# Performance work log

Measured on AMD Instinct MI355X. Metric: run time of the kernel, lower is better.

## Reference

```python
import jax, jax.numpy as jnp
import numpy as np

# Constants matching the module / repo call convention:
# self.tensor2points(x, self.voxel_size) -> offset := init voxel_size, voxel_size := default
OFFSET = np.array([0.1, 0.1, 0.2], dtype=np.float32)      # init_kwargs voxel_size (used as offset)
VOX    = np.array([0.05, 0.05, 0.1], dtype=np.float32)    # tensor2points default voxel_size
BIG = 1e10  # cross-batch distance sentinel


def setup_inputs() -> dict:
    key = jax.random.key(0)
    k1, k2, k3, k4, k5 = jax.random.split(key, 5)
    m, n, C = 4096, 32768, 64
    # sparse voxel indices: (batch, z, y, x) over KITTI grid [40, 1600, 1408]
    zi = jax.random.randint(k1, (m, 1), 0, 40, dtype=jnp.int32)
    yi = jax.random.randint(k2, (m, 1), 0, 1600, dtype=jnp.int32)
    xi = jax.random.randint(k3, (m, 1), 0, 1408, dtype=jnp.int32)
    bi = jnp.zeros((m, 1), dtype=jnp.int32)
    x_indices = jnp.concatenate([bi, zi, yi, xi], axis=1)
    x_features = jax.random.normal(k4, (m, C), dtype=jnp.float32)
    # unknown points: bxyz in KITTI range x:[0,70.4] y:[-40,40] z:[-3,1]
    u = jax.random.uniform(k5, (n, 3), dtype=jnp.float32)
    lo = jnp.array([0.0, -40.0, -3.0], dtype=jnp.float32)
    hi = jnp.array([70.4, 40.0, 1.0], dtype=jnp.float32)
    xyz = lo + u * (hi - lo)
    points_mean = jnp.concatenate([jnp.zeros((n, 1), jnp.float32), xyz], axis=1)
    return {"x_features": x_features, "x_indices": x_indices, "points_mean": points_mean}


def reference(x_features, x_indices, points_mean):
    # tensor2points: voxel index (b,z,y,x) -> world bxyz
    idxf = x_indices.astype(jnp.float32)
    vox = jnp.asarray(VOX)
    off = jnp.asarray(OFFSET)
    known_xyz = idxf[:, jnp.array([3, 2, 1])] * vox + off + 0.5 * vox   # (m,3)
    known_b = idxf[:, 0]                                                # (m,)
    unk_b = points_mean[:, 0]                                           # (n,)
    unk_xyz = points_mean[:, 1:4]                                       # (n,3)
    # brute-force squared distances (pointnet2 three_nn returns squared dists)
    d2 = jnp.sum((unk_xyz[:, None, :] - known_xyz[None, :, :]) ** 2, axis=-1)  # (n,m)
    d2 = jnp.where(unk_b[:, None] == known_b[None, :], d2, jnp.float32(BIG))
    neg, idx = jax.lax.top_k(-d2, 3)        # 3 nearest neighbors
    dist = -neg                              # (n,3)
    dist_recip = 1.0 / (dist + 1e-8)
    weight = dist_recip / jnp.sum(dist_recip, axis=1, keepdims=True)    # (n,3)
    # three_interpolate: gather + weighted sum
    interpolated = jnp.sum(x_features[idx] * weight[..., None], axis=1)  # (n,C)
    return interpolated
```

## Files before the change

kernel.cpp:

```cpp
#include <hip/hip_runtime.h>


#define NXC 24
#define NYC 27
#define NCC (NXC * NYC)
#define WCELL 3.0f
#define NBB 16

__device__ __forceinline__ void ins_lex(float d, int j,
                                        float& a0, float& a1, float& a2,
                                        int& i0, int& i1, int& i2) {
    bool c0 = (d < a0) || (d == a0 && j < i0);
    bool c1 = (d < a1) || (d == a1 && j < i1);
    bool c2 = (d < a2) || (d == a2 && j < i2);
    float nb1 = c0 ? a0 : (c1 ? d : a1);
    int   nj1 = c0 ? i0 : (c1 ? j : i1);
    float nb2 = c1 ? a1 : (c2 ? d : a2);
    int   nj2 = c1 ? i1 : (c2 ? j : i2);
    a0 = c0 ? d : a0; i0 = c0 ? j : i0;
    a1 = nb1; i1 = nj1; a2 = nb2; i2 = nj2;
}

__device__ __forceinline__ int kcell_of(int4 v) {
    float kx = ((float)v.w * 0.05f + 0.1f) + 0.025f;
    float ky = ((float)v.z * 0.05f + 0.1f) + 0.025f;
    int ix = min(NXC - 1, max(0, (int)(kx * (1.0f / WCELL))));
    int iy = min(NYC - 1, max(0, (int)(ky * (1.0f / WCELL))));
    return iy * NXC + ix;
}

__device__ __forceinline__ int qcell_of(float qx, float qy) {
    int ix = min(NXC - 1, max(0, (int)floorf(qx * (1.0f / WCELL))));
    int iy = min(NYC - 1, max(0, (int)floorf(qy * (1.0f / WCELL))));
    return iy * NXC + ix;
}

__global__ __launch_bounds__(1024) void prep_fused(const int4* __restrict__ xind4,
                                                   const float* __restrict__ pts,
                                                   float4* __restrict__ tab,
                                                   float4* __restrict__ qpts,
                                                   int* __restrict__ cs_g,
                                                   int m, int n) {
#pragma clang fp contract(off)
    __shared__ int hAK[NCC], hAQ[NCC];
    __shared__ int hPK[NCC], hPQ[NCC];
    __shared__ int bk[NCC], bq[NCC];
    __shared__ int wsk[16], wsq[16];
    const int t = threadIdx.x, b = blockIdx.x;
    for (int i = t; i < NCC; i += 1024) { hAK[i] = 0; hAQ[i] = 0; hPK[i] = 0; hPQ[i] = 0; }
    __syncthreads();

    const int tot = m + n;
    const int chunk = (tot + NBB - 1) / NBB;
    const int e0 = b * chunk;
    const int e1 = min(e0 + chunk, tot);

    for (int base = 0; base < m; base += 4096) {
        int4 v[4];
#pragma unroll
        for (int k = 0; k < 4; ++k) {
            int j = base + k * 1024 + t;
            v[k] = xind4[min(j, m - 1)];
        }
#pragma unroll
        for (int k = 0; k < 4; ++k) {
            int j = base + k * 1024 + t;
            if (j < m) {
                int cell = kcell_of(v[k]);
                atomicAdd(&hAK[cell], 1);
                if (j < e0) atomicAdd(&hPK[cell], 1);
            }
        }
    }
    for (int base = 0; base < n; base += 4096) {
        float4 u[4];
#pragma unroll
        for (int k = 0; k < 4; ++k) {
            int qi = base + k * 1024 + t;
            u[k] = ((const float4*)pts)[min(qi, n - 1)];
        }
#pragma unroll
        for (int k = 0; k < 4; ++k) {
            int qi = base + k * 1024 + t;
            if (qi < n) {
                int cell = qcell_of(u[k].y, u[k].z);
                atomicAdd(&hAQ[cell], 1);
                if (m + qi < e0) atomicAdd(&hPQ[cell], 1);
            }
        }
    }
    __syncthreads();

    int ownK = 0, ownQ = 0, vk = 0, vq = 0;
    if (t < NCC) { ownK = hAK[t]; ownQ = hAQ[t]; vk = ownK; vq = ownQ; }
#pragma unroll
    for (int d = 1; d < 64; d <<= 1) {
        int ok = __shfl_up(vk, d, 64);
        int oq = __shfl_up(vq, d, 64);
        if ((t & 63) >= d) { vk += ok; vq += oq; }
    }
    if ((t & 63) == 63) { wsk[t >> 6] = vk; wsq[t >> 6] = vq; }
    __syncthreads();
    if (t < 64) {
        int ok0 = (t < 16) ? wsk[t] : 0;
        int oq0 = (t < 16) ? wsq[t] : 0;
        int sk = ok0, sq = oq0;
#pragma unroll
        for (int d = 1; d < 16; d <<= 1) {
            int ok = __shfl_up(sk, d, 64);
            int oq = __shfl_up(sq, d, 64);
            if (t >= d) { sk += ok; sq += oq; }
        }
        if (t < 16) { wsk[t] = sk - ok0; wsq[t] = sq - oq0; }
    }
    __syncthreads();
    if (t < NCC) {
        int exK = vk + wsk[t >> 6] - ownK;
        int exQ = vq + wsq[t >> 6] - ownQ;
        bk[t] = exK + hPK[t];
        bq[t] = exQ + hPQ[t];
        if (b == 0) cs_g[t] = exK;
    }
    if (b == 0 && t == 0) cs_g[NCC] = m;
    __syncthreads();

    for (int i = t; i < NCC; i += 1024) { hPK[i] = 0; hPQ[i] = 0; }
    __syncthreads();

    for (int e = e0 + t; e < e1; e += 1024) {
        if (e < m) {
            int4 v = xind4[e];
            float kx = ((float)v.w * 0.05f + 0.1f) + 0.025f;
            float ky = ((float)v.z * 0.05f + 0.1f) + 0.025f;
            float kz = ((float)v.y * 0.1f  + 0.2f) + 0.05f;
            int cell = kcell_of(v);
            int r = atomicAdd(&hPK[cell], 1);
            tab[bk[cell] + r] = make_float4(kx, ky, kz, __int_as_float(e));
        } else {
            int q = e - m;
            float4 u = ((const float4*)pts)[q];
            int cell = qcell_of(u.y, u.z);
            int r = atomicAdd(&hPQ[cell], 1);
            qpts[bq[cell] + r] = make_float4(__int_as_float(q), u.y, u.z, u.w);
        }
    }
}

__global__ __launch_bounds__(256) void scan3nn(const float4* __restrict__ tab,
                                               const int* __restrict__ cs,
                                               const float4* __restrict__ qpts,
                                               const float* __restrict__ feats,
                                               float* __restrict__ out,
                                               int m, int n, int C) {
#pragma clang fp contract(off)
    __shared__ int cs_lds[NCC + 1];
    const int t = threadIdx.x;
    for (int i = t; i < NCC + 1; i += 256) cs_lds[i] = cs[i];
    __syncthreads();

    const int sub = t & 3;
    const int gid = blockIdx.x * 64 + (t >> 2);
    const float INF = __builtin_huge_valf();
    if (gid >= n) return;

    const float4 rec = qpts[gid];
    const int q = __float_as_int(rec.x);
    const float qx = rec.y, qy = rec.z, qz = rec.w;

    float a0 = INF, a1 = INF, a2 = INF;
    int   i0 = 0x7fffffff, i1 = 0x7fffffff, i2 = 0x7fffffff;
    float T = INF;

    const int cx = min(NXC - 1, max(0, (int)floorf(qx * (1.0f / WCELL))));
    const int cy = min(NYC - 1, max(0, (int)floorf(qy * (1.0f / WCELL))));

    auto scan_span = [&](int s0, int s1) {
        for (int s = s0 + sub; s < s1; s += 4) {
            float4 kp = tab[s];
            float dx = qx - kp.x, dy = qy - kp.y, dz = qz - kp.z;
            float d = dx * dx + dy * dy;
            d = d + dz * dz;
            ins_lex(d, __float_as_int(kp.w), a0, a1, a2, i0, i1, i2);
        }
    };
    auto tighten = [&]() {
        float tg = a2;
        tg = fminf(tg, __shfl_xor(tg, 1, 4));
        tg = fminf(tg, __shfl_xor(tg, 2, 4));
        T = tg;
    };
    auto row_mdy2 = [&](int iy) {
        float cyl = (float)iy * WCELL;
        float mdy = fmaxf(fmaxf(cyl - qy, qy - (cyl + WCELL)), 0.f);
        return mdy * mdy;
    };
    auto row_scan = [&](int iy, int excl_lo, int excl_hi) -> bool {
        float mdy2 = row_mdy2(iy);
        float Ts = T * 1.0001f + 1e-4f;
        if (mdy2 > Ts) return false;
        float rem = fmaxf(Ts - mdy2, 0.f);
        float rx = fminf(sqrtf(rem), 1000.0f);
        int ixlo = max(0, (int)floorf((qx - rx) * (1.0f / WCELL)) - 1);
        int ixhi = min(NXC - 1, (int)floorf((qx + rx) * (1.0f / WCELL)) + 1);
        const int rowb = iy * NXC;
        if (excl_lo <= excl_hi) {
            int h1 = min(ixhi, excl_lo - 1);
            if (ixlo <= h1) scan_span(cs_lds[rowb + ixlo], cs_lds[rowb + h1 + 1]);
            int l2 = max(ixlo, excl_hi + 1);
            if (l2 <= ixhi) scan_span(cs_lds[rowb + l2], cs_lds[rowb + ixhi + 1]);
        } else {
            scan_span(cs_lds[rowb + ixlo], cs_lds[rowb + ixhi + 1]);
        }
        tighten();
        return true;
    };

    const int lo0 = max(0, cx - 1), hi0 = min(NXC - 1, cx + 1);
    scan_span(cs_lds[cy * NXC + lo0], cs_lds[cy * NXC + hi0 + 1]);
    tighten();
    row_scan(cy, lo0, hi0);
    bool up = true, dn = true;
    for (int o = 1; (up || dn) && o < NYC; ++o) {
        if (up) { int iy = cy + o; up = (iy < NYC) && row_scan(iy, 1, 0); }
        if (dn) { int iy = cy - o; dn = (iy >= 0) && row_scan(iy, 1, 0); }
    }

    for (int mlane = 1; mlane < 4; mlane <<= 1) {
        float b0 = __shfl_xor(a0, mlane, 4);
        float b1 = __shfl_xor(a1, mlane, 4);
        float b2 = __shfl_xor(a2, mlane, 4);
        int   j0 = __shfl_xor(i0, mlane, 4);
        int   j1 = __shfl_xor(i1, mlane, 4);
        int   j2 = __shfl_xor(i2, mlane, 4);
        ins_lex(b0, j0, a0, a1, a2, i0, i1, i2);
        ins_lex(b1, j1, a0, a1, a2, i0, i1, i2);
        ins_lex(b2, j2, a0, a1, a2, i0, i1, i2);
    }

    float r0 = 1.0f / (a0 + 1e-8f);
    float r1 = 1.0f / (a1 + 1e-8f);
    float r2 = 1.0f / (a2 + 1e-8f);
    float s  = r0 + r1 + r2;
    const float w0 = r0 / s, w1 = r1 / s, w2 = r2 / s;

    const int nf4 = C >> 2;
    const float4* F  = (const float4*)feats;
    const float4* F0 = F + (size_t)min(i0, m - 1) * nf4;
    const float4* F1 = F + (size_t)min(i1, m - 1) * nf4;
    const float4* F2 = F + (size_t)min(i2, m - 1) * nf4;
    float4* O = (float4*)out + (size_t)q * nf4;
    for (int c = sub; c < nf4; c += 4) {
        float4 a = F0[c], b = F1[c], cc = F2[c];
        float4 o;
        o.x = w0 * a.x + w1 * b.x + w2 * cc.x;
        o.y = w0 * a.y + w1 * b.y + w2 * cc.y;
        o.z = w0 * a.z + w1 * b.z + w2 * cc.z;
        o.w = w0 * a.w + w1 * b.w + w2 * cc.w;
        O[c] = o;
    }
}

extern "C" void kernel_launch(void* const* d_in, const int* in_sizes, int n_in,
                              void* d_out, int out_size, void* d_ws, size_t ws_size,
                              hipStream_t stream) {
    const float* feats = (const float*)d_in[0];
    const int4*  xind4 = (const int4*)d_in[1];
    const float* pts   = (const float*)d_in[2];
    float*       out   = (float*)d_out;

    const int m = in_sizes[1] / 4;
    const int n = in_sizes[2] / 4;
    const int C = in_sizes[0] / m;

    const size_t off_tab  = 0;
    const size_t off_cs   = off_tab  + (size_t)m * 16;
    const size_t off_qpts = off_cs   + (size_t)(NCC + 1) * 4;
    const size_t need     = off_qpts + (size_t)n * 16;

    if (ws_size >= need && m >= 3 && (C & 3) == 0) {
        char* ws = (char*)d_ws;
        float4* tab  = (float4*)(ws + off_tab);
        int*    cs   = (int*)(ws + off_cs);
        float4* qpts = (float4*)(ws + off_qpts);

        prep_fused<<<NBB, 1024, 0, stream>>>(xind4, pts, tab, qpts, cs, m, n);
        const int nb = (n + 63) / 64;
        scan3nn<<<nb, 256, 0, stream>>>(tab, cs, qpts, feats, out, m, n, C);
    }
}
```

Baseline: 42.55 us.

## Pack histogram counters into one atomic and use 8 lanes per query

The prep kernel now packs the total and prefix cell counts into a single 32-bit LDS atomic (low and high 16 bits) when m and n are below 65536, which halves the atomics in the histogram pass. The query histogram loop is unrolled to 8 loads per thread. The search kernel splits each query across 8 lanes instead of 4, with 32 queries per block, and widens the shuffles to match. More lanes per query adds parallelism and grid size but also adds shuffle and merge overhead, and lanes go idle when cells hold few points.

```diff
diff --git a/kernel.cpp b/kernel.cpp
--- a/kernel.cpp
+++ b/kernel.cpp
@@ -35,6 +35,7 @@
     return iy * NXC + ix;
 }
 
+template <bool PACKED>
 __global__ __launch_bounds__(1024) void prep_fused(const int4* __restrict__ xind4,
                                                    const float* __restrict__ pts,
                                                    float4* __restrict__ tab,
@@ -42,12 +43,12 @@
                                                    int* __restrict__ cs_g,
                                                    int m, int n) {
 #pragma clang fp contract(off)
-    __shared__ int hAK[NCC], hAQ[NCC];
+    __shared__ int hK[NCC], hQ[NCC];
     __shared__ int hPK[NCC], hPQ[NCC];
     __shared__ int bk[NCC], bq[NCC];
     __shared__ int wsk[16], wsq[16];
     const int t = threadIdx.x, b = blockIdx.x;
-    for (int i = t; i < NCC; i += 1024) { hAK[i] = 0; hAQ[i] = 0; hPK[i] = 0; hPQ[i] = 0; }
+    for (int i = t; i < NCC; i += 1024) { hK[i] = 0; hQ[i] = 0; hPK[i] = 0; hPQ[i] = 0; }
     __syncthreads();
 
     const int tot = m + n;
@@ -67,32 +68,49 @@
             int j = base + k * 1024 + t;
             if (j < m) {
                 int cell = kcell_of(v[k]);
-                atomicAdd(&hAK[cell], 1);
-                if (j < e0) atomicAdd(&hPK[cell], 1);
+                if constexpr (PACKED) {
+                    atomicAdd(&hK[cell], (j < e0) ? 0x10001 : 1);
+                } else {
+                    atomicAdd(&hK[cell], 1);
+                    if (j < e0) atomicAdd(&hPK[cell], 1);
+                }
             }
         }
     }
-    for (int base = 0; base < n; base += 4096) {
-        float4 u[4];
-#pragma unroll
-        for (int k = 0; k < 4; ++k) {
+    for (int base = 0; base < n; base += 8192) {
+        float4 u[8];
+#pragma unroll
+        for (int k = 0; k < 8; ++k) {
             int qi = base + k * 1024 + t;
             u[k] = ((const float4*)pts)[min(qi, n - 1)];
         }
 #pragma unroll
-        for (int k = 0; k < 4; ++k) {
+        for (int k = 0; k < 8; ++k) {
             int qi = base + k * 1024 + t;
             if (qi < n) {
                 int cell = qcell_of(u[k].y, u[k].z);
-                atomicAdd(&hAQ[cell], 1);
-                if (m + qi < e0) atomicAdd(&hPQ[cell], 1);
+                if constexpr (PACKED) {
+                    atomicAdd(&hQ[cell], (m + qi < e0) ? 0x10001 : 1);
+                } else {
+                    atomicAdd(&hQ[cell], 1);
+                    if (m + qi < e0) atomicAdd(&hPQ[cell], 1);
+                }
             }
         }
     }
     __syncthreads();
 
-    int ownK = 0, ownQ = 0, vk = 0, vq = 0;
-    if (t < NCC) { ownK = hAK[t]; ownQ = hAQ[t]; vk = ownK; vq = ownQ; }
+    int ownK = 0, ownQ = 0, preK = 0, preQ = 0, vk = 0, vq = 0;
+    if (t < NCC) {
+        if constexpr (PACKED) {
+            ownK = hK[t] & 0xffff;  preK = ((unsigned)hK[t]) >> 16;
+            ownQ = hQ[t] & 0xffff;  preQ = ((unsigned)hQ[t]) >> 16;
+        } else {
+            ownK = hK[t]; preK = hPK[t];
+            ownQ = hQ[t]; preQ = hPQ[t];
+        }
+        vk = ownK; vq = ownQ;
+    }
 #pragma unroll
     for (int d = 1; d < 64; d <<= 1) {
         int ok = __shfl_up(vk, d, 64);
@@ -117,8 +135,8 @@
     if (t < NCC) {
         int exK = vk + wsk[t >> 6] - ownK;
         int exQ = vq + wsq[t >> 6] - ownQ;
-        bk[t] = exK + hPK[t];
-        bq[t] = exQ + hPQ[t];
+        bk[t] = exK + preK;
+        bq[t] = exQ + preQ;
         if (b == 0) cs_g[t] = exK;
     }
     if (b == 0 && t == 0) cs_g[NCC] = m;
@@ -158,8 +176,8 @@
     for (int i = t; i < NCC + 1; i += 256) cs_lds[i] = cs[i];
     __syncthreads();
 
-    const int sub = t & 3;
-    const int gid = blockIdx.x * 64 + (t >> 2);
+    const int sub = t & 7;
+    const int gid = blockIdx.x * 32 + (t >> 3);
     const float INF = __builtin_huge_valf();
     if (gid >= n) return;
 
@@ -175,7 +193,7 @@
     const int cy = min(NYC - 1, max(0, (int)floorf(qy * (1.0f / WCELL))));
 
     auto scan_span = [&](int s0, int s1) {
-        for (int s = s0 + sub; s < s1; s += 4) {
+        for (int s = s0 + sub; s < s1; s += 8) {
             float4 kp = tab[s];
             float dx = qx - kp.x, dy = qy - kp.y, dz = qz - kp.z;
             float d = dx * dx + dy * dy;
@@ -185,8 +203,9 @@
     };
     auto tighten = [&]() {
         float tg = a2;
-        tg = fminf(tg, __shfl_xor(tg, 1, 4));
-        tg = fminf(tg, __shfl_xor(tg, 2, 4));
+        tg = fminf(tg, __shfl_xor(tg, 1, 8));
+        tg = fminf(tg, __shfl_xor(tg, 2, 8));
+        tg = fminf(tg, __shfl_xor(tg, 4, 8));
         T = tg;
     };
     auto row_mdy2 = [&](int iy) {
@@ -225,13 +244,13 @@
         if (dn) { int iy = cy - o; dn = (iy >= 0) && row_scan(iy, 1, 0); }
     }
 
-    for (int mlane = 1; mlane < 4; mlane <<= 1) {
-        float b0 = __shfl_xor(a0, mlane, 4);
-        float b1 = __shfl_xor(a1, mlane, 4);
-        float b2 = __shfl_xor(a2, mlane, 4);
-        int   j0 = __shfl_xor(i0, mlane, 4);
-        int   j1 = __shfl_xor(i1, mlane, 4);
-        int   j2 = __shfl_xor(i2, mlane, 4);
+    for (int mlane = 1; mlane < 8; mlane <<= 1) {
+        float b0 = __shfl_xor(a0, mlane, 8);
+        float b1 = __shfl_xor(a1, mlane, 8);
+        float b2 = __shfl_xor(a2, mlane, 8);
+        int   j0 = __shfl_xor(i0, mlane, 8);
+        int   j1 = __shfl_xor(i1, mlane, 8);
+        int   j2 = __shfl_xor(i2, mlane, 8);
         ins_lex(b0, j0, a0, a1, a2, i0, i1, i2);
         ins_lex(b1, j1, a0, a1, a2, i0, i1, i2);
         ins_lex(b2, j2, a0, a1, a2, i0, i1, i2);
@@ -249,7 +268,7 @@
     const float4* F1 = F + (size_t)min(i1, m - 1) * nf4;
     const float4* F2 = F + (size_t)min(i2, m - 1) * nf4;
     float4* O = (float4*)out + (size_t)q * nf4;
-    for (int c = sub; c < nf4; c += 4) {
+    for (int c = sub; c < nf4; c += 8) {
         float4 a = F0[c], b = F1[c], cc = F2[c];
         float4 o;
         o.x = w0 * a.x + w1 * b.x + w2 * cc.x;
@@ -283,8 +302,12 @@
         int*    cs   = (int*)(ws + off_cs);
         float4* qpts = (float4*)(ws + off_qpts);
 
-        prep_fused<<<NBB, 1024, 0, stream>>>(xind4, pts, tab, qpts, cs, m, n);
-        const int nb = (n + 63) / 64;
+        if (m < 65536 && n < 65536) {
+            prep_fused<true><<<NBB, 1024, 0, stream>>>(xind4, pts, tab, qpts, cs, m, n);
+        } else {
+            prep_fused<false><<<NBB, 1024, 0, stream>>>(xind4, pts, tab, qpts, cs, m, n);
+        }
+        const int nb = (n + 31) / 32;
         scan3nn<<<nb, 256, 0, stream>>>(tab, cs, qpts, feats, out, m, n, C);
     }
 }
```

Result: faster. 38.24 us (-10.1%).
